# Kernel optimization log

Measured on AMD Instinct MI355X. Metric: run time of the kernel, lower is better.

Reference implementation:

```python
import jax, jax.numpy as jnp
import numpy as np

M = 262144          # total lanes
N_GROUPS = 32768    # unique obstacle ids (static; original uses torch.unique)
H = 64              # lane_hidden_size
I = 64              # lane_info_enc_size
F = 64              # lane_future_enc_size
SOFT_ARGMAX_DEGREE = 1.0


def setup_inputs() -> dict:
    key = jax.random.key(0)
    k = jax.random.split(key, 8)
    lane_ht = jax.random.normal(k[0], (M, H), jnp.float32)
    lane_info_enc = jax.random.normal(k[1], (M, I), jnp.float32)
    lane_future_enc = jax.random.normal(k[2], (M, F), jnp.float32)
    # sorted group ids covering every group (8 lanes per obstacle)
    same_obstacle_mask = jnp.sort(jnp.arange(M, dtype=jnp.int32) % N_GROUPS).reshape(M, 1)
    # lane_scoring_mlp params: Linear(128->16) + ReLU + Linear(16->1)
    W1 = jax.random.normal(k[3], (H + I, 16), jnp.float32) * 0.05
    b1 = jnp.zeros((16,), jnp.float32)
    W2 = jax.random.normal(k[4], (16, 1), jnp.float32) * 0.05
    b2 = jnp.zeros((1,), jnp.float32)
    return {"lane_ht": lane_ht, "lane_info_enc": lane_info_enc,
            "lane_future_enc": lane_future_enc,
            "W1": W1, "b1": b1, "W2": W2, "b2": b2,
            "same_obstacle_mask": same_obstacle_mask}


def reference(lane_ht, lane_info_enc, lane_future_enc, W1, b1, W2, b2, same_obstacle_mask):
    seg = same_obstacle_mask.reshape(-1)                       # [M] int group ids
    # per-lane score via small MLP
    x = jnp.concatenate([lane_ht, lane_info_enc], axis=1)      # [M, 128]
    h = jax.nn.relu(x @ W1 + b1)                               # [M, 16]
    score = (h @ W2 + b2).reshape(-1) * SOFT_ARGMAX_DEGREE     # [M]
    # per-group (segment) softmax -- exact math of the dense MxN min/max/exp/sum emulation
    smax = jax.lax.stop_gradient(
        jax.ops.segment_max(score, seg, num_segments=N_GROUPS))  # [N]
    e = jnp.exp(score - smax[seg])                             # [M]
    denom = jax.ops.segment_sum(e, seg, num_segments=N_GROUPS)  # [N]
    prob = e / denom[seg]                                      # [M]
    # softmax-weighted per-group pooling of concatenated encodings
    total = jnp.concatenate([lane_ht, lane_info_enc, lane_future_enc], axis=1)  # [M, 192]
    return jax.ops.segment_sum(total * prob[:, None], seg, num_segments=N_GROUPS)  # [N, 192]
```

## Files before the change

### kernel.cpp

```cpp
#include <hip/hip_runtime.h>


#define LPG 8
#define GROUPS_PER_BLOCK 32

__global__ __launch_bounds__(256) void lane_attn_kernel(
    const float* __restrict__ ht,
    const float* __restrict__ info,
    const float* __restrict__ fut,
    const float* __restrict__ W1,
    const float* __restrict__ b1,
    const float* __restrict__ W2,
    const float* __restrict__ b2,
    const int*   __restrict__ seg,
    float*       __restrict__ out)
{
    __shared__ float sprob[256];
    __shared__ int   sgid[GROUPS_PER_BLOCK];

    const int t         = threadIdx.x;
    const int blockBase = blockIdx.x * 256;
    const int lane      = blockBase + t;

    float h[16];
#pragma unroll
    for (int j = 0; j < 16; ++j) h[j] = b1[j];

    const float4* htp = (const float4*)(ht   + (size_t)lane * 64);
    const float4* inp = (const float4*)(info + (size_t)lane * 64);

#pragma unroll 4
    for (int k4 = 0; k4 < 16; ++k4) {
        float4 v = htp[k4];
#pragma unroll
        for (int j = 0; j < 16; ++j) {
            h[j] = fmaf(v.x, W1[(k4 * 4 + 0) * 16 + j], h[j]);
            h[j] = fmaf(v.y, W1[(k4 * 4 + 1) * 16 + j], h[j]);
            h[j] = fmaf(v.z, W1[(k4 * 4 + 2) * 16 + j], h[j]);
            h[j] = fmaf(v.w, W1[(k4 * 4 + 3) * 16 + j], h[j]);
        }
    }
#pragma unroll 4
    for (int k4 = 0; k4 < 16; ++k4) {
        float4 v = inp[k4];
#pragma unroll
        for (int j = 0; j < 16; ++j) {
            h[j] = fmaf(v.x, W1[(64 + k4 * 4 + 0) * 16 + j], h[j]);
            h[j] = fmaf(v.y, W1[(64 + k4 * 4 + 1) * 16 + j], h[j]);
            h[j] = fmaf(v.z, W1[(64 + k4 * 4 + 2) * 16 + j], h[j]);
            h[j] = fmaf(v.w, W1[(64 + k4 * 4 + 3) * 16 + j], h[j]);
        }
    }

    float score = b2[0];
#pragma unroll
    for (int j = 0; j < 16; ++j)
        score = fmaf(fmaxf(h[j], 0.0f), W2[j], score);

    float m = score;
    m = fmaxf(m, __shfl_xor(m, 1));
    m = fmaxf(m, __shfl_xor(m, 2));
    m = fmaxf(m, __shfl_xor(m, 4));
    float e = __expf(score - m);
    float s = e;
    s += __shfl_xor(s, 1);
    s += __shfl_xor(s, 2);
    s += __shfl_xor(s, 4);
    sprob[t] = e / s;

    if (t < GROUPS_PER_BLOCK) sgid[t] = seg[blockBase + t * LPG];
    __syncthreads();

    const int wave = t >> 6;
    const int c    = t & 63;
    for (int gg = 0; gg < 8; ++gg) {
        const int gl  = wave * 8 + gg;
        const int gid = sgid[gl];
        const int r0  = blockBase + gl * LPG;
        float a0 = 0.0f, a1 = 0.0f, a2 = 0.0f;
#pragma unroll
        for (int i = 0; i < LPG; ++i) {
            const float  p = sprob[gl * LPG + i];
            const size_t r = (size_t)(r0 + i) * 64;
            a0 = fmaf(p, ht[r + c],   a0);
            a1 = fmaf(p, info[r + c], a1);
            a2 = fmaf(p, fut[r + c],  a2);
        }
        float* o = out + (size_t)gid * 192;
        o[c]       = a0;
        o[64 + c]  = a1;
        o[128 + c] = a2;
    }
}

extern "C" void kernel_launch(void* const* d_in, const int* in_sizes, int n_in,
                              void* d_out, int out_size, void* d_ws, size_t ws_size,
                              hipStream_t stream) {
    const float* ht   = (const float*)d_in[0];
    const float* info = (const float*)d_in[1];
    const float* fut  = (const float*)d_in[2];
    const float* W1   = (const float*)d_in[3];
    const float* b1   = (const float*)d_in[4];
    const float* W2   = (const float*)d_in[5];
    const float* b2   = (const float*)d_in[6];
    const int*   seg  = (const int*)d_in[7];
    float*       out  = (float*)d_out;

    const int M = in_sizes[7];
    const int blocks = M / 256;

    lane_attn_kernel<<<blocks, 256, 0, stream>>>(ht, info, fut, W1, b1, W2, b2,
                                                 seg, out);
}
```

Baseline: 222.5 us.

## Stage lane rows through skewed shared-memory tile for coalesced loads and reuse

```diff
diff --git a/kernel.cpp b/kernel.cpp
--- a/kernel.cpp
+++ b/kernel.cpp
@@ -1,8 +1,5 @@
 #include <hip/hip_runtime.h>
 
-
-#define LPG 8
-#define GROUPS_PER_BLOCK 32
 
 __global__ __launch_bounds__(256) void lane_attn_kernel(
     const float* __restrict__ ht,
@@ -15,40 +12,69 @@
     const int*   __restrict__ seg,
     float*       __restrict__ out)
 {
-    __shared__ float sprob[256];
-    __shared__ int   sgid[GROUPS_PER_BLOCK];
+    __shared__ float tile[256 * 64];
 
     const int t         = threadIdx.x;
     const int blockBase = blockIdx.x * 256;
-    const int lane      = blockBase + t;
 
     float h[16];
 #pragma unroll
     for (int j = 0; j < 16; ++j) h[j] = b1[j];
 
-    const float4* htp = (const float4*)(ht   + (size_t)lane * 64);
-    const float4* inp = (const float4*)(info + (size_t)lane * 64);
-
-#pragma unroll 4
-    for (int k4 = 0; k4 < 16; ++k4) {
-        float4 v = htp[k4];
+    {
+        const float4* src = (const float4*)ht + (size_t)blockBase * 16;
 #pragma unroll
-        for (int j = 0; j < 16; ++j) {
-            h[j] = fmaf(v.x, W1[(k4 * 4 + 0) * 16 + j], h[j]);
-            h[j] = fmaf(v.y, W1[(k4 * 4 + 1) * 16 + j], h[j]);
-            h[j] = fmaf(v.z, W1[(k4 * 4 + 2) * 16 + j], h[j]);
-            h[j] = fmaf(v.w, W1[(k4 * 4 + 3) * 16 + j], h[j]);
+        for (int it = 0; it < 16; ++it) {
+            const int f = it * 256 + t;
+            float4 v = src[f];
+            const int r  = f >> 4;
+            const int c0 = (f & 15) << 2;
+            const int rb = r * 64;
+            tile[rb + ((c0 + 0 + r) & 63)] = v.x;
+            tile[rb + ((c0 + 1 + r) & 63)] = v.y;
+            tile[rb + ((c0 + 2 + r) & 63)] = v.z;
+            tile[rb + ((c0 + 3 + r) & 63)] = v.w;
         }
     }
-#pragma unroll 4
-    for (int k4 = 0; k4 < 16; ++k4) {
-        float4 v = inp[k4];
+    __syncthreads();
+
+    {
+        const int rb = t * 64;
+#pragma unroll 8
+        for (int k = 0; k < 64; ++k) {
+            const float x = tile[rb + ((k + t) & 63)];
 #pragma unroll
-        for (int j = 0; j < 16; ++j) {
-            h[j] = fmaf(v.x, W1[(64 + k4 * 4 + 0) * 16 + j], h[j]);
-            h[j] = fmaf(v.y, W1[(64 + k4 * 4 + 1) * 16 + j], h[j]);
-            h[j] = fmaf(v.z, W1[(64 + k4 * 4 + 2) * 16 + j], h[j]);
-            h[j] = fmaf(v.w, W1[(64 + k4 * 4 + 3) * 16 + j], h[j]);
+            for (int j = 0; j < 16; ++j)
+                h[j] = fmaf(x, W1[k * 16 + j], h[j]);
+        }
+    }
+    __syncthreads();
+
+    {
+        const float4* src = (const float4*)info + (size_t)blockBase * 16;
+#pragma unroll
+        for (int it = 0; it < 16; ++it) {
+            const int f = it * 256 + t;
+            float4 v = src[f];
+            const int r  = f >> 4;
+            const int c0 = (f & 15) << 2;
+            const int rb = r * 64;
+            tile[rb + ((c0 + 0 + r) & 63)] = v.x;
+            tile[rb + ((c0 + 1 + r) & 63)] = v.y;
+            tile[rb + ((c0 + 2 + r) & 63)] = v.z;
+            tile[rb + ((c0 + 3 + r) & 63)] = v.w;
+        }
+    }
+    __syncthreads();
+
+    {
+        const int rb = t * 64;
+#pragma unroll 8
+        for (int k = 0; k < 64; ++k) {
+            const float x = tile[rb + ((k + t) & 63)];
+#pragma unroll
+            for (int j = 0; j < 16; ++j)
+                h[j] = fmaf(x, W1[(64 + k) * 16 + j], h[j]);
         }
     }
 
@@ -66,25 +92,23 @@
     s += __shfl_xor(s, 1);
     s += __shfl_xor(s, 2);
     s += __shfl_xor(s, 4);
-    sprob[t] = e / s;
-
-    if (t < GROUPS_PER_BLOCK) sgid[t] = seg[blockBase + t * LPG];
-    __syncthreads();
+    const float prob = e / s;
 
     const int wave = t >> 6;
     const int c    = t & 63;
     for (int gg = 0; gg < 8; ++gg) {
-        const int gl  = wave * 8 + gg;
-        const int gid = sgid[gl];
-        const int r0  = blockBase + gl * LPG;
+        const int lr0 = wave * 64 + gg * 8;
+        const int r0g = blockBase + lr0;
+        const int gid = seg[r0g];
         float a0 = 0.0f, a1 = 0.0f, a2 = 0.0f;
 #pragma unroll
-        for (int i = 0; i < LPG; ++i) {
-            const float  p = sprob[gl * LPG + i];
-            const size_t r = (size_t)(r0 + i) * 64;
-            a0 = fmaf(p, ht[r + c],   a0);
-            a1 = fmaf(p, info[r + c], a1);
-            a2 = fmaf(p, fut[r + c],  a2);
+        for (int i = 0; i < 8; ++i) {
+            const float p  = __shfl(prob, gg * 8 + i);
+            const int   lr = lr0 + i;
+            const size_t rg = (size_t)(r0g + i) * 64;
+            a0 = fmaf(p, ht[rg + c], a0);
+            a1 = fmaf(p, tile[lr * 64 + ((c + lr) & 63)], a1);
+            a2 = fmaf(p, fut[rg + c], a2);
         }
         float* o = out + (size_t)gid * 192;
         o[c]       = a0;
```

Result: slower. 232.4 us (+4.5%).
